# Performance work log

Hardware: AMD Instinct MI355X
Metric: run time of the kernel (lower is better)

Reference implementation:

```python
import jax, jax.numpy as jnp
import numpy as np

B, G, IN, H, OUT = 4096, 8, 512, 1024, 64


def setup_inputs() -> dict:
    key = jax.random.key(0)
    k0, k1, k2, k3 = jax.random.split(key, 4)
    x = jax.random.normal(k0, (B, IN), dtype=jnp.float32)
    gid = jax.random.randint(k1, (B,), 0, G, dtype=jnp.int32)
    # Per-group 2-layer MLP params (Kaiming-ish scaling)
    W1 = jax.random.normal(k2, (G, IN, H), dtype=jnp.float32) / np.sqrt(IN)
    b1 = jnp.zeros((G, H), dtype=jnp.float32)
    W2 = jax.random.normal(k3, (G, H, OUT), dtype=jnp.float32) / np.sqrt(H)
    b2 = jnp.zeros((G, OUT), dtype=jnp.float32)
    return {"x": x, "gid": gid, "W1": W1, "b1": b1, "W2": W2, "b2": b2}


def reference(x, gid, W1, b1, W2, b2):
    # Routed 2-layer MLP: each sample i uses expert head gid[i].
    # Compute all G group GEMMs (grouped-GEMM style), then select the
    # routed row per sample with a one-hot contraction (no [B,IN,H]
    # per-sample weight materialization).
    onehot = jax.nn.one_hot(gid, W1.shape[0], dtype=x.dtype)  # [B, G]
    h_all = jnp.einsum('bi,gih->bgh', x, W1) + b1[None]       # [B, G, H]
    h = jax.nn.relu(jnp.einsum('bgh,bg->bh', h_all, onehot))  # [B, H]
    y_all = jnp.einsum('bh,gho->bgo', h, W2) + b2[None]       # [B, G, OUT]
    y = jnp.einsum('bgo,bg->bo', y_all, onehot)               # [B, OUT]
    return y
```

## Files before the change

kernel.cpp:

```cpp
#include <hip/hip_runtime.h>
#include <hip/hip_bf16.h>

#define B_ 4096
#define G_ 8
#define IN_ 512
#define H_ 1024
#define OUT_ 64
#define MAXT64 72
#define MAXT32 136

typedef float f32x4 __attribute__((ext_vector_type(4)));
typedef __bf16 bf16x8 __attribute__((ext_vector_type(8)));
typedef unsigned short u16x8 __attribute__((ext_vector_type(8)));

__device__ inline unsigned short f2bf(float f) {
  unsigned int u = __builtin_bit_cast(unsigned int, f);
  u += 0x7fffu + ((u >> 16) & 1u);
  return (unsigned short)(u >> 16);
}

__device__ inline u16x8 pack8(float4 a, float4 b) {
  return u16x8{f2bf(a.x), f2bf(a.y), f2bf(a.z), f2bf(a.w),
               f2bf(b.x), f2bf(b.y), f2bf(b.z), f2bf(b.w)};
}

__device__ inline bool tile_lookup(const int* __restrict__ meta, int mt,
                                   int shift, int& g, int& row0, int& start,
                                   int& cnt) {
  int ts = 0;
  bool found = false;
#pragma unroll
  for (int gg = 0; gg < G_; gg++) {
    int s = meta[gg], e = meta[gg + 1];
    int T = (e - s + (1 << shift) - 1) >> shift;
    if (!found && mt >= ts && mt < ts + T) {
      g = gg;
      row0 = (mt - ts) << shift;
      start = s;
      cnt = e - s;
      found = true;
    }
    ts += T;
  }
  return found;
}

__global__ __launch_bounds__(256) void prep_kernel(
    const float* __restrict__ W1, const float* __restrict__ W2,
    const float* __restrict__ x, const int* __restrict__ gid,
    unsigned short* __restrict__ W1t, unsigned short* __restrict__ W2t,
    unsigned short* __restrict__ xb, int* __restrict__ meta,
    int* __restrict__ perm) {
  int b = blockIdx.x;
  int t = threadIdx.x;
  if (b < 4096) {
    __shared__ float tile[32][33];
    int h32 = b & 31, k32 = (b >> 5) & 15, g = b >> 9;
    int kl = t >> 3, nl = (t & 7) * 4;
    const float* src =
        W1 + ((size_t)g * IN_ + k32 * 32 + kl) * H_ + h32 * 32 + nl;
    float4 v = *(const float4*)src;
    tile[kl][nl + 0] = v.x;
    tile[kl][nl + 1] = v.y;
    tile[kl][nl + 2] = v.z;
    tile[kl][nl + 3] = v.w;
    __syncthreads();
    int nl2 = t >> 3, kl2 = (t & 7) * 4;
    ushort4 o;
    o.x = f2bf(tile[kl2 + 0][nl2]);
    o.y = f2bf(tile[kl2 + 1][nl2]);
    o.z = f2bf(tile[kl2 + 2][nl2]);
    o.w = f2bf(tile[kl2 + 3][nl2]);
    *(ushort4*)(W1t + ((size_t)g * H_ + h32 * 32 + nl2) * IN_ + k32 * 32 +
                kl2) = o;
  } else if (b < 4608) {
    __shared__ float tile2[32][33];
    int bb = b - 4096;
    int g = bb >> 6, k32 = (bb >> 1) & 31, n32 = bb & 1;
    int kl = t >> 3, nl = (t & 7) * 4;
    const float* src =
        W2 + ((size_t)g * H_ + k32 * 32 + kl) * OUT_ + n32 * 32 + nl;
    float4 v = *(const float4*)src;
    tile2[kl][nl + 0] = v.x;
    tile2[kl][nl + 1] = v.y;
    tile2[kl][nl + 2] = v.z;
    tile2[kl][nl + 3] = v.w;
    __syncthreads();
    int nl2 = t >> 3, kl2 = (t & 7) * 4;
    ushort4 o;
    o.x = f2bf(tile2[kl2 + 0][nl2]);
    o.y = f2bf(tile2[kl2 + 1][nl2]);
    o.z = f2bf(tile2[kl2 + 2][nl2]);
    o.w = f2bf(tile2[kl2 + 3][nl2]);
    *(ushort4*)(W2t + ((size_t)g * OUT_ + n32 * 32 + nl2) * H_ + k32 * 32 +
                kl2) = o;
  } else if (b < 5632) {
    int bb = b - 4608;
    size_t base = (size_t)bb * 2048 + t * 8;
    float4 v0 = *(const float4*)(x + base);
    float4 v1 = *(const float4*)(x + base + 4);
    *(u16x8*)(xb + base) = pack8(v0, v1);
  } else {
    __shared__ unsigned short lc[G_][256];
    __shared__ int offs_s[G_ + 1];
#pragma unroll
    for (int g = 0; g < G_; g++) lc[g][t] = 0;
    int myg[16];
    const int base = t * 16;
    __syncthreads();
#pragma unroll
    for (int j = 0; j < 16; j++) {
      myg[j] = gid[base + j];
      lc[myg[j]][t]++;
    }
    __syncthreads();
    {
      int g = t >> 5, k = t & 31;
      unsigned short pref[8];
      int s = 0;
#pragma unroll
      for (int j = 0; j < 8; j++) {
        pref[j] = (unsigned short)s;
        s += lc[g][8 * k + j];
      }
      int incl = s;
#pragma unroll
      for (int d = 1; d < 32; d <<= 1) {
        int o = __shfl_up(incl, d, 32);
        if (k >= d) incl += o;
      }
      int excl = incl - s;
      if (k == 31) offs_s[g + 1] = incl;
#pragma unroll
      for (int j = 0; j < 8; j++)
        lc[g][8 * k + j] = (unsigned short)(excl + pref[j]);
    }
    __syncthreads();
    if (t == 0) {
      int o = 0;
      for (int g = 0; g < G_; g++) {
        int c = offs_s[g + 1];
        offs_s[g] = o;
        meta[g] = o;
        o += c;
      }
      offs_s[G_] = o;
      meta[G_] = o;
    }
    __syncthreads();
    int cur[G_];
#pragma unroll
    for (int g = 0; g < G_; g++) cur[g] = offs_s[g] + (int)lc[g][t];
#pragma unroll
    for (int j = 0; j < 16; j++) {
      int g = myg[j];
      perm[cur[g]++] = base + j;
    }
  }
}

__global__ __launch_bounds__(256) void gemm1_kernel(
    const unsigned short* __restrict__ xb,
    const unsigned short* __restrict__ W1t, const float* __restrict__ b1,
    const int* __restrict__ meta, const int* __restrict__ perm,
    unsigned short* __restrict__ hb) {
  int b = blockIdx.x;
  int mt = b >> 4, nt = b & 15;
  int g, row0, start, cnt;
  if (!tile_lookup(meta, mt, 5, g, row0, start, cnt)) return;
  int n0 = nt * 64;

  __shared__ __attribute__((aligned(16))) unsigned short As[2][32 * 64];
  __shared__ __attribute__((aligned(16))) unsigned short Bs[2][64 * 64];
  __shared__ int rows[32];

  int tid = threadIdx.x;
  int lane = tid & 63;
  int wv = tid >> 6;

  if (tid < 32) rows[tid] = perm[start + min(row0 + tid, cnt - 1)];
  __syncthreads();

  int r = tid >> 3, cc = tid & 7;
  const unsigned short* xsrc = xb + (size_t)rows[r] * IN_ + cc * 8;
  int aoff = r * 64 + ((cc ^ (r & 7)) << 3);

  int brow0 = wv * 16 + (lane >> 3);
  int brow1 = brow0 + 8;
  int bsl = lane & 7;
  const unsigned short* bsrc0 = W1t + ((size_t)g * H_ + n0 + brow0) * IN_ +
                                ((bsl ^ (brow0 & 7)) << 3);
  const unsigned short* bsrc1 = W1t + ((size_t)g * H_ + n0 + brow1) * IN_ +
                                ((bsl ^ (brow1 & 7)) << 3);
  int boff0 = wv * 1024 + lane * 8;
  int boff1 = wv * 1024 + 512 + lane * 8;

  int fl = lane & 15, q = lane >> 4;
  int m0 = (wv >> 1) * 16, nw = (wv & 1) * 32;
  int apA = (m0 + fl) * 64;
  int bpA = (nw + fl) * 64;
  int bpB = (nw + 16 + fl) * 64;

  f32x4 acc[2];
  acc[0] = f32x4{0.f, 0.f, 0.f, 0.f};
  acc[1] = f32x4{0.f, 0.f, 0.f, 0.f};

  u16x8 aR[8], bR0[8], bR1[8];
#pragma unroll
  for (int it = 0; it < 8; it++) {
    int k0 = it * 64;
    aR[it] = *(const u16x8*)(xsrc + k0);
    bR0[it] = *(const u16x8*)(bsrc0 + k0);
    bR1[it] = *(const u16x8*)(bsrc1 + k0);
  }

  *(u16x8*)&As[0][aoff] = aR[0];
  *(u16x8*)&Bs[0][boff0] = bR0[0];
  *(u16x8*)&Bs[0][boff1] = bR1[0];
  __syncthreads();

  for (int it = 0; it < 8; it++) {
    int p = it & 1;
    if (it < 7) {
      *(u16x8*)&As[p ^ 1][aoff] = aR[it + 1];
      *(u16x8*)&Bs[p ^ 1][boff0] = bR0[it + 1];
      *(u16x8*)&Bs[p ^ 1][boff1] = bR1[it + 1];
    }
#pragma unroll
    for (int s = 0; s < 2; s++) {
      int off = (((s << 2) + q) ^ (fl & 7)) << 3;
      bf16x8 a0 = *(const bf16x8*)&As[p][apA + off];
      bf16x8 fb0 = *(const bf16x8*)&Bs[p][bpA + off];
      bf16x8 fb1 = *(const bf16x8*)&Bs[p][bpB + off];
      acc[0] = __builtin_amdgcn_mfma_f32_16x16x32_bf16(a0, fb0, acc[0], 0, 0, 0);
      acc[1] = __builtin_amdgcn_mfma_f32_16x16x32_bf16(a0, fb1, acc[1], 0, 0, 0);
    }
    __syncthreads();
  }

#pragma unroll
  for (int ni = 0; ni < 2; ni++) {
    int col = n0 + nw + ni * 16 + fl;
    float bias = b1[g * H_ + col];
#pragma unroll
    for (int rg = 0; rg < 4; rg++) {
      int rl = m0 + q * 4 + rg;
      if (row0 + rl < cnt) {
        float v = fmaxf(acc[ni][rg] + bias, 0.f);
        hb[(size_t)(start + row0 + rl) * H_ + col] = f2bf(v);
      }
    }
  }
}

__global__ __launch_bounds__(256) void gemm2_kernel(
    const unsigned short* __restrict__ hb,
    const unsigned short* __restrict__ W2t, const float* __restrict__ b2,
    const int* __restrict__ meta, const int* __restrict__ perm,
    float* __restrict__ y) {
  int mt = blockIdx.x;
  int g, row0, start, cnt;
  if (!tile_lookup(meta, mt, 6, g, row0, start, cnt)) return;

  __shared__ __attribute__((aligned(16))) unsigned short As2[2][64 * 128];
  __shared__ __attribute__((aligned(16))) unsigned short Bs2[2][64 * 128];
  __shared__ int rows[64];

  int tid = threadIdx.x;
  int lane = tid & 63;
  int wv = tid >> 6;

  if (tid < 64) rows[tid] = perm[start + min(row0 + tid, cnt - 1)];

  int arow_in_op = lane >> 4;
  int asl = lane & 15;
  const unsigned short* asrc[4];
  int adst[4];
#pragma unroll
  for (int j = 0; j < 4; j++) {
    int row = wv * 16 + j * 4 + arow_in_op;
    int cs = asl ^ (row & 7);
    asrc[j] =
        hb + (size_t)(start + min(row0 + row, cnt - 1)) * H_ + (cs << 3);
    adst[j] = (wv * 16 + j * 4) * 128 + lane * 8;
  }

  int bn = tid >> 2, qd = tid & 3;
  const unsigned short* bsrc = W2t + ((size_t)g * OUT_ + bn) * H_ + qd * 32;
  int bdst[4];
#pragma unroll
  for (int j = 0; j < 4; j++) {
    int ch = 4 * qd + j;
    bdst[j] = bn * 128 + ((ch ^ (bn & 7)) << 3);
  }

  int fl = lane & 15, q = lane >> 4;
  int m0 = (wv >> 1) * 32, nw = (wv & 1) * 32;
  int apA = (m0 + fl) * 128;
  int apB = (m0 + 16 + fl) * 128;
  int bpA = (nw + fl) * 128;
  int bpB = (nw + 16 + fl) * 128;

  f32x4 acc[2][2];
#pragma unroll
  for (int i = 0; i < 2; i++)
#pragma unroll
    for (int j = 0; j < 2; j++) acc[i][j] = f32x4{0.f, 0.f, 0.f, 0.f};

  u16x8 av[4], bv[4];
#pragma unroll
  for (int j = 0; j < 4; j++) av[j] = *(const u16x8*)(asrc[j] + 0);
#pragma unroll
  for (int j = 0; j < 4; j++) bv[j] = *(const u16x8*)(bsrc + j * 8);
  __syncthreads();
#pragma unroll
  for (int j = 0; j < 4; j++) *(u16x8*)&As2[0][adst[j]] = av[j];
#pragma unroll
  for (int j = 0; j < 4; j++) *(u16x8*)&Bs2[0][bdst[j]] = bv[j];
#pragma unroll
  for (int j = 0; j < 4; j++) av[j] = *(const u16x8*)(asrc[j] + 128);
#pragma unroll
  for (int j = 0; j < 4; j++) bv[j] = *(const u16x8*)(bsrc + 128 + j * 8);
  __syncthreads();

  for (int it = 0; it < 8; it++) {
    int p = it & 1;
    if (it < 7) {
#pragma unroll
      for (int j = 0; j < 4; j++) *(u16x8*)&As2[p ^ 1][adst[j]] = av[j];
#pragma unroll
      for (int j = 0; j < 4; j++) *(u16x8*)&Bs2[p ^ 1][bdst[j]] = bv[j];
    }
    if (it < 6) {
      int kn = (it + 2) * 128;
#pragma unroll
      for (int j = 0; j < 4; j++) av[j] = *(const u16x8*)(asrc[j] + kn);
#pragma unroll
      for (int j = 0; j < 4; j++)
        bv[j] = *(const u16x8*)(bsrc + kn + j * 8);
    }
#pragma unroll
    for (int s = 0; s < 4; s++) {
      int off = (((s << 2) + q) ^ (fl & 7)) << 3;
      bf16x8 a0 = *(const bf16x8*)&As2[p][apA + off];
      bf16x8 a1 = *(const bf16x8*)&As2[p][apB + off];
      bf16x8 fb0 = *(const bf16x8*)&Bs2[p][bpA + off];
      bf16x8 fb1 = *(const bf16x8*)&Bs2[p][bpB + off];
      acc[0][0] = __builtin_amdgcn_mfma_f32_16x16x32_bf16(a0, fb0, acc[0][0], 0, 0, 0);
      acc[1][0] = __builtin_amdgcn_mfma_f32_16x16x32_bf16(a1, fb0, acc[1][0], 0, 0, 0);
      acc[0][1] = __builtin_amdgcn_mfma_f32_16x16x32_bf16(a0, fb1, acc[0][1], 0, 0, 0);
      acc[1][1] = __builtin_amdgcn_mfma_f32_16x16x32_bf16(a1, fb1, acc[1][1], 0, 0, 0);
    }
    __syncthreads();
  }

#pragma unroll
  for (int ni = 0; ni < 2; ni++) {
    int col = nw + ni * 16 + fl;
    float bias = b2[g * OUT_ + col];
#pragma unroll
    for (int mi = 0; mi < 2; mi++) {
#pragma unroll
      for (int rg = 0; rg < 4; rg++) {
        int rl = m0 + mi * 16 + q * 4 + rg;
        if (row0 + rl < cnt) {
          y[(size_t)rows[rl] * OUT_ + col] = acc[mi][ni][rg] + bias;
        }
      }
    }
  }
}

extern "C" void kernel_launch(void* const* d_in, const int* in_sizes, int n_in,
                              void* d_out, int out_size, void* d_ws,
                              size_t ws_size, hipStream_t stream) {
  const float* x = (const float*)d_in[0];
  const int* gid = (const int*)d_in[1];
  const float* W1 = (const float*)d_in[2];
  const float* b1 = (const float*)d_in[3];
  const float* W2 = (const float*)d_in[4];
  const float* b2 = (const float*)d_in[5];
  float* y = (float*)d_out;

  int* meta = (int*)d_ws;
  int* perm = (int*)((char*)d_ws + 64);
  unsigned short* W1t = (unsigned short*)((char*)d_ws + (1u << 16));
  unsigned short* W2t = (unsigned short*)((char*)d_ws + (16u << 20));
  unsigned short* xb = (unsigned short*)((char*)d_ws + (24u << 20));
  unsigned short* hb = (unsigned short*)((char*)d_ws + (32u << 20));

  prep_kernel<<<5633, 256, 0, stream>>>(W1, W2, x, gid, W1t, W2t, xb, meta,
                                        perm);
  gemm1_kernel<<<MAXT32 * 16, 256, 0, stream>>>(xb, W1t, b1, meta, perm, hb);
  gemm2_kernel<<<MAXT64, 256, 0, stream>>>(hb, W2t, b2, meta, perm, y);
}
```

Baseline: 109.9 us.

## Use K=128 tiles with rolling register prefetch in gemm1

The gemm1 K-loop now uses 128-wide tiles (4 iterations instead of 8), which halves the number of barriers. The old code loaded the whole K range into registers up front; the new code prefetches one tile ahead into a register buffer, so far fewer registers stay live. B loads are reorganized so each thread fetches 64 contiguous bytes of one W1t row. This costs twice the shared memory per block, which may reduce occupancy.

Measured after the change: 114.5 us. 4.2% more time.

```diff
diff --git a/kernel.cpp b/kernel.cpp
--- a/kernel.cpp
+++ b/kernel.cpp
@@ -170,8 +170,8 @@
   if (!tile_lookup(meta, mt, 5, g, row0, start, cnt)) return;
   int n0 = nt * 64;
 
-  __shared__ __attribute__((aligned(16))) unsigned short As[2][32 * 64];
-  __shared__ __attribute__((aligned(16))) unsigned short Bs[2][64 * 64];
+  __shared__ __attribute__((aligned(16))) unsigned short As[2][32 * 128];
+  __shared__ __attribute__((aligned(16))) unsigned short Bs[2][64 * 128];
   __shared__ int rows[32];
 
   int tid = threadIdx.x;
@@ -181,59 +181,72 @@
   if (tid < 32) rows[tid] = perm[start + min(row0 + tid, cnt - 1)];
   __syncthreads();
 
-  int r = tid >> 3, cc = tid & 7;
-  const unsigned short* xsrc = xb + (size_t)rows[r] * IN_ + cc * 8;
-  int aoff = r * 64 + ((cc ^ (r & 7)) << 3);
-
-  int brow0 = wv * 16 + (lane >> 3);
-  int brow1 = brow0 + 8;
-  int bsl = lane & 7;
-  const unsigned short* bsrc0 = W1t + ((size_t)g * H_ + n0 + brow0) * IN_ +
-                                ((bsl ^ (brow0 & 7)) << 3);
-  const unsigned short* bsrc1 = W1t + ((size_t)g * H_ + n0 + brow1) * IN_ +
-                                ((bsl ^ (brow1 & 7)) << 3);
-  int boff0 = wv * 1024 + lane * 8;
-  int boff1 = wv * 1024 + 512 + lane * 8;
+  int r = tid >> 3, c2 = (tid & 7) * 2;
+  const unsigned short* xsrc = xb + (size_t)rows[r] * IN_;
+  int asl0 = c2 ^ (r & 7);
+  int asl1 = (c2 + 1) ^ (r & 7);
+  int aoff0 = r * 128 + (asl0 << 3);
+  int aoff1 = r * 128 + (asl1 << 3);
+
+  int bn = tid >> 2, qd = tid & 3;
+  const unsigned short* bsrc =
+      W1t + ((size_t)g * H_ + n0 + bn) * IN_ + qd * 32;
+  int bdst[4];
+#pragma unroll
+  for (int j = 0; j < 4; j++) {
+    int ch = 4 * qd + j;
+    bdst[j] = bn * 128 + (((ch ^ (bn & 7)) & 15) << 3);
+  }
 
   int fl = lane & 15, q = lane >> 4;
   int m0 = (wv >> 1) * 16, nw = (wv & 1) * 32;
-  int apA = (m0 + fl) * 64;
-  int bpA = (nw + fl) * 64;
-  int bpB = (nw + 16 + fl) * 64;
+  int apA = (m0 + fl) * 128;
+  int bpA = (nw + fl) * 128;
+  int bpB = (nw + 16 + fl) * 128;
 
   f32x4 acc[2];
   acc[0] = f32x4{0.f, 0.f, 0.f, 0.f};
   acc[1] = f32x4{0.f, 0.f, 0.f, 0.f};
 
-  u16x8 aR[8], bR0[8], bR1[8];
-#pragma unroll
-  for (int it = 0; it < 8; it++) {
-    int k0 = it * 64;
-    aR[it] = *(const u16x8*)(xsrc + k0);
-    bR0[it] = *(const u16x8*)(bsrc0 + k0);
-    bR1[it] = *(const u16x8*)(bsrc1 + k0);
-  }
-
-  *(u16x8*)&As[0][aoff] = aR[0];
-  *(u16x8*)&Bs[0][boff0] = bR0[0];
-  *(u16x8*)&Bs[0][boff1] = bR1[0];
+  u16x8 a0r = *(const u16x8*)(xsrc + c2 * 8);
+  u16x8 a1r = *(const u16x8*)(xsrc + c2 * 8 + 8);
+  u16x8 bv[4];
+#pragma unroll
+  for (int j = 0; j < 4; j++) bv[j] = *(const u16x8*)(bsrc + j * 8);
+  *(u16x8*)&As[0][aoff0] = a0r;
+  *(u16x8*)&As[0][aoff1] = a1r;
+#pragma unroll
+  for (int j = 0; j < 4; j++) *(u16x8*)&Bs[0][bdst[j]] = bv[j];
+  a0r = *(const u16x8*)(xsrc + 128 + c2 * 8);
+  a1r = *(const u16x8*)(xsrc + 128 + c2 * 8 + 8);
+#pragma unroll
+  for (int j = 0; j < 4; j++) bv[j] = *(const u16x8*)(bsrc + 128 + j * 8);
   __syncthreads();
 
-  for (int it = 0; it < 8; it++) {
+  for (int it = 0; it < 4; it++) {
     int p = it & 1;
-    if (it < 7) {
-      *(u16x8*)&As[p ^ 1][aoff] = aR[it + 1];
-      *(u16x8*)&Bs[p ^ 1][boff0] = bR0[it + 1];
-      *(u16x8*)&Bs[p ^ 1][boff1] = bR1[it + 1];
-    }
-#pragma unroll
-    for (int s = 0; s < 2; s++) {
+    if (it < 3) {
+      *(u16x8*)&As[p ^ 1][aoff0] = a0r;
+      *(u16x8*)&As[p ^ 1][aoff1] = a1r;
+#pragma unroll
+      for (int j = 0; j < 4; j++) *(u16x8*)&Bs[p ^ 1][bdst[j]] = bv[j];
+    }
+    if (it < 2) {
+      int kn = (it + 2) * 128;
+      a0r = *(const u16x8*)(xsrc + kn + c2 * 8);
+      a1r = *(const u16x8*)(xsrc + kn + c2 * 8 + 8);
+#pragma unroll
+      for (int j = 0; j < 4; j++)
+        bv[j] = *(const u16x8*)(bsrc + kn + j * 8);
+    }
+#pragma unroll
+    for (int s = 0; s < 4; s++) {
       int off = (((s << 2) + q) ^ (fl & 7)) << 3;
-      bf16x8 a0 = *(const bf16x8*)&As[p][apA + off];
+      bf16x8 a = *(const bf16x8*)&As[p][apA + off];
       bf16x8 fb0 = *(const bf16x8*)&Bs[p][bpA + off];
       bf16x8 fb1 = *(const bf16x8*)&Bs[p][bpB + off];
-      acc[0] = __builtin_amdgcn_mfma_f32_16x16x32_bf16(a0, fb0, acc[0], 0, 0, 0);
-      acc[1] = __builtin_amdgcn_mfma_f32_16x16x32_bf16(a0, fb1, acc[1], 0, 0, 0);
+      acc[0] = __builtin_amdgcn_mfma_f32_16x16x32_bf16(a, fb0, acc[0], 0, 0, 0);
+      acc[1] = __builtin_amdgcn_mfma_f32_16x16x32_bf16(a, fb1, acc[1], 0, 0, 0);
     }
     __syncthreads();
   }
```
